# Optimization experiments

Measured on AMD Instinct MI355X. Metric: run time of the kernel, lower is better.

The kernel has to match this reference:

```python
import jax, jax.numpy as jnp
import numpy as np

SR = 24000
BLOCK = 0.4
OVERLAP = 0.7
FRAME = int(BLOCK * SR)                # 9600
SHIFT = int(BLOCK * SR * (1 - OVERLAP))
GAMMA_A = -70.0
ALPHA = 1e-4
EPS = 1e-8


def measure_loudness(sig):
    # sig: [N, T] flattened (batch*bands) envelope signals
    N, T = sig.shape
    n_frames = (T - FRAME) // SHIFT + 1
    # unfold: overlapping windows [n_frames, FRAME] of sample indices
    win_idx = jnp.arange(n_frames)[:, None] * SHIFT + jnp.arange(FRAME)[None, :]
    # mean-square energy per window (== sum(x^2)/frame_size in torch) -> [N, n_frames]
    z = jnp.mean(sig[:, win_idx] ** 2, axis=-1)
    el = -0.691 + 10.0 * jnp.log10(z + EPS)
    # absolute gating
    idx_a = (el > GAMMA_A).astype(z.dtype)
    z_ave_a = jnp.sum(z * idx_a, axis=1, keepdims=True) / (jnp.sum(idx_a, axis=1, keepdims=True) + EPS)
    # relative gating 10 dB below gated loudness
    gamma_r = -0.691 + 10.0 * jnp.log10(z_ave_a + EPS) - 10.0
    idx_ar = idx_a * (el > gamma_r).astype(z.dtype)
    z_ave_ar = jnp.sum(z * idx_ar, axis=1, keepdims=True) / (jnp.sum(idx_ar, axis=1, keepdims=True) + EPS)
    lufs = -0.691 + 10.0 * jnp.log10(z_ave_ar + EPS)  # [N, 1]
    return lufs


def setup_inputs() -> dict:
    key = jax.random.key(0)
    k1, k2 = jax.random.split(key)
    B, C, T = 16, 32, 192000  # batch, auditory bands, 8 s @ 24 kHz
    x_env = 0.1 * jax.random.normal(k1, (B, C, T), dtype=jnp.float32)
    y_env = 0.1 * jax.random.normal(k2, (B, C, T), dtype=jnp.float32)
    return {"x_env": x_env, "y_env": y_env}


def reference(x_env, y_env):
    B, C, T = x_env.shape
    loud_x = measure_loudness(x_env.reshape(B * C, T))
    loud_y = measure_loudness(y_env.reshape(B * C, T))
    level_loss = ALPHA * jnp.sum(jnp.maximum(loud_y - loud_x, 0.0))
    return level_loss
```

## Files before the change

### kernel.cpp

```cpp
#include <hip/hip_runtime.h>

constexpr int T_LEN    = 192000;
constexpr int N_SIG    = 512;
constexpr int FRAME    = 9600;
constexpr int SHIFT    = 2880;
constexpr int SUB      = 960;
constexpr int NFRAMES  = (T_LEN - FRAME) / SHIFT + 1;
constexpr int SUB_PER_SHIFT = SHIFT / SUB;
constexpr int SUB_PER_FRAME = FRAME / SUB;
constexpr int NSUB     = (NFRAMES - 1) * SUB_PER_SHIFT + SUB_PER_FRAME;
constexpr int F4_PER_SUB = SUB / 4;

typedef float f32x4 __attribute__((ext_vector_type(4)));

__device__ __forceinline__ float wave_reduce_f32(float v) {
    #pragma unroll
    for (int off = 32; off > 0; off >>= 1) v += __shfl_xor(v, off);
    return v;
}

__device__ __forceinline__ double wave_reduce_f64(double v) {
    #pragma unroll
    for (int off = 32; off > 0; off >>= 1) v += __shfl_xor(v, off);
    return v;
}

__global__ __launch_bounds__(256) void dhaspi_loudness_kernel(
    const float* __restrict__ x, const float* __restrict__ y,
    float* __restrict__ lufs_out)
{
    const int bid  = blockIdx.x;
    const int p    = bid >> 9;
    const int n    = bid & (N_SIG - 1);
    const float* sig = (p == 0 ? x : y) + (size_t)n * T_LEN;
    const f32x4* sig4 = reinterpret_cast<const f32x4*>(sig);

    __shared__ float s_sub[NSUB];

    const int tid  = threadIdx.x;
    const int wave = tid >> 6;
    const int lane = tid & 63;

    for (int k = wave; k < NSUB; k += 4) {
        float acc = 0.0f;
        const int base = k * F4_PER_SUB;
        #pragma unroll
        for (int i = 0; i < 4; ++i) {
            int idx = i * 64 + lane;
            if (idx < F4_PER_SUB) {
                f32x4 v = __builtin_nontemporal_load(&sig4[base + idx]);
                acc += v.x * v.x + v.y * v.y + v.z * v.z + v.w * v.w;
            }
        }
        acc = wave_reduce_f32(acc);
        if (lane == 0) s_sub[k] = acc;
    }
    __syncthreads();

    if (wave == 0) {
        float zs = 0.0f;
        const int b0 = lane * SUB_PER_SHIFT;
        #pragma unroll
        for (int j = 0; j < SUB_PER_FRAME; ++j) zs += s_sub[b0 + j];
        const double z  = (double)zs / (double)FRAME;
        const double el = -0.691 + 10.0 * log10(z + 1e-8);

        const double ia = (el > -70.0) ? 1.0 : 0.0;
        double sz = wave_reduce_f64(z * ia);
        double si = wave_reduce_f64(ia);
        const double z_ave_a = sz / (si + 1e-8);

        const double gamma_r = -0.691 + 10.0 * log10(z_ave_a + 1e-8) - 10.0;
        const double iar = ia * ((el > gamma_r) ? 1.0 : 0.0);
        double sz2 = wave_reduce_f64(z * iar);
        double si2 = wave_reduce_f64(iar);
        const double z_ave_ar = sz2 / (si2 + 1e-8);

        const double lufs = -0.691 + 10.0 * log10(z_ave_ar + 1e-8);
        if (lane == 0) lufs_out[bid] = (float)lufs;
    }
}

__global__ __launch_bounds__(512) void dhaspi_loss_kernel(
    const float* __restrict__ lufs, float* __restrict__ out)
{
    const int tid  = threadIdx.x;
    const int wave = tid >> 6;
    const int lane = tid & 63;

    const float lx = lufs[tid];
    const float ly = lufs[N_SIG + tid];
    const float d  = ly - lx;
    double v = (d > 0.0f) ? (double)d : 0.0;
    v = wave_reduce_f64(v);

    __shared__ double s[8];
    if (lane == 0) s[wave] = v;
    __syncthreads();
    if (tid == 0) {
        double t = 0.0;
        #pragma unroll
        for (int i = 0; i < 8; ++i) t += s[i];
        out[0] = (float)(1e-4 * t);
    }
}

extern "C" void kernel_launch(void* const* d_in, const int* in_sizes, int n_in,
                              void* d_out, int out_size, void* d_ws, size_t ws_size,
                              hipStream_t stream) {
    const float* x = (const float*)d_in[0];
    const float* y = (const float*)d_in[1];
    float* lufs = (float*)d_ws;
    float* out  = (float*)d_out;

    dhaspi_loudness_kernel<<<2 * N_SIG, 256, 0, stream>>>(x, y, lufs);
    dhaspi_loss_kernel<<<1, 512, 0, stream>>>(lufs, out);
}
```

Measured before the change: 120.2 us.

## Fuse loudness and loss kernels with last-block atomic reduction

Merges the per-signal loudness kernel and the final hinge-sum kernel into one launch. Each 512-thread block handles both the x and y signal for one index, so the grid is 512 blocks instead of 1024. The last block to finish, found through an atomic counter, does the final reduction. This removes one kernel launch and the intermediate lufs round-trip, but adds a memset launch and halves the block count, which may cut parallelism across CUs.

```diff
diff --git a/kernel.cpp b/kernel.cpp
--- a/kernel.cpp
+++ b/kernel.cpp
@@ -10,6 +10,7 @@
 constexpr int SUB_PER_FRAME = FRAME / SUB;
 constexpr int NSUB     = (NFRAMES - 1) * SUB_PER_SHIFT + SUB_PER_FRAME;
 constexpr int F4_PER_SUB = SUB / 4;
+constexpr int NWAVES   = 8;
 
 typedef float f32x4 __attribute__((ext_vector_type(4)));
 
@@ -25,23 +26,10 @@
     return v;
 }
 
-__global__ __launch_bounds__(256) void dhaspi_loudness_kernel(
-    const float* __restrict__ x, const float* __restrict__ y,
-    float* __restrict__ lufs_out)
+__device__ double block_lufs(const f32x4* __restrict__ sig4,
+                             int wave, int lane, float* s_sub)
 {
-    const int bid  = blockIdx.x;
-    const int p    = bid >> 9;
-    const int n    = bid & (N_SIG - 1);
-    const float* sig = (p == 0 ? x : y) + (size_t)n * T_LEN;
-    const f32x4* sig4 = reinterpret_cast<const f32x4*>(sig);
-
-    __shared__ float s_sub[NSUB];
-
-    const int tid  = threadIdx.x;
-    const int wave = tid >> 6;
-    const int lane = tid & 63;
-
-    for (int k = wave; k < NSUB; k += 4) {
+    for (int k = wave; k < NSUB; k += NWAVES) {
         float acc = 0.0f;
         const int base = k * F4_PER_SUB;
         #pragma unroll
@@ -57,6 +45,7 @@
     }
     __syncthreads();
 
+    double lufs = 0.0;
     if (wave == 0) {
         float zs = 0.0f;
         const int b0 = lane * SUB_PER_SHIFT;
@@ -76,32 +65,56 @@
         double si2 = wave_reduce_f64(iar);
         const double z_ave_ar = sz2 / (si2 + 1e-8);
 
-        const double lufs = -0.691 + 10.0 * log10(z_ave_ar + 1e-8);
-        if (lane == 0) lufs_out[bid] = (float)lufs;
+        lufs = -0.691 + 10.0 * log10(z_ave_ar + 1e-8);
     }
+    __syncthreads();
+    return lufs;
 }
 
-__global__ __launch_bounds__(512) void dhaspi_loss_kernel(
-    const float* __restrict__ lufs, float* __restrict__ out)
+__global__ __launch_bounds__(512) void dhaspi_fused_kernel(
+    const float* __restrict__ x, const float* __restrict__ y,
+    double* __restrict__ hinge_ws,
+    unsigned int* __restrict__ cnt,
+    float* __restrict__ out)
 {
+    const int n    = blockIdx.x;
     const int tid  = threadIdx.x;
     const int wave = tid >> 6;
     const int lane = tid & 63;
 
-    const float lx = lufs[tid];
-    const float ly = lufs[N_SIG + tid];
-    const float d  = ly - lx;
-    double v = (d > 0.0f) ? (double)d : 0.0;
-    v = wave_reduce_f64(v);
+    __shared__ float s_sub[NSUB];
+    __shared__ bool  s_win;
 
-    __shared__ double s[8];
-    if (lane == 0) s[wave] = v;
+    const f32x4* x4 = reinterpret_cast<const f32x4*>(x + (size_t)n * T_LEN);
+    const f32x4* y4 = reinterpret_cast<const f32x4*>(y + (size_t)n * T_LEN);
+
+    const double lx = block_lufs(x4, wave, lane, s_sub);
+    const double ly = block_lufs(y4, wave, lane, s_sub);
+
+    if (tid == 0) {
+        double h = ly - lx;
+        h = (h > 0.0) ? h : 0.0;
+        __hip_atomic_store(&hinge_ws[n], h, __ATOMIC_RELAXED,
+                           __HIP_MEMORY_SCOPE_AGENT);
+        unsigned int old = __hip_atomic_fetch_add(cnt, 1u, __ATOMIC_ACQ_REL,
+                                                  __HIP_MEMORY_SCOPE_AGENT);
+        s_win = (old == (unsigned int)(gridDim.x - 1));
+    }
     __syncthreads();
-    if (tid == 0) {
-        double t = 0.0;
-        #pragma unroll
-        for (int i = 0; i < 8; ++i) t += s[i];
-        out[0] = (float)(1e-4 * t);
+
+    if (s_win) {
+        double v = __hip_atomic_load(&hinge_ws[tid], __ATOMIC_RELAXED,
+                                     __HIP_MEMORY_SCOPE_AGENT);
+        v = wave_reduce_f64(v);
+        __shared__ double sd[NWAVES];
+        if (lane == 0) sd[wave] = v;
+        __syncthreads();
+        if (tid == 0) {
+            double t = 0.0;
+            #pragma unroll
+            for (int i = 0; i < NWAVES; ++i) t += sd[i];
+            out[0] = (float)(1e-4 * t);
+        }
     }
 }
 
@@ -110,9 +123,11 @@
                               hipStream_t stream) {
     const float* x = (const float*)d_in[0];
     const float* y = (const float*)d_in[1];
-    float* lufs = (float*)d_ws;
-    float* out  = (float*)d_out;
+    float* out = (float*)d_out;
 
-    dhaspi_loudness_kernel<<<2 * N_SIG, 256, 0, stream>>>(x, y, lufs);
-    dhaspi_loss_kernel<<<1, 512, 0, stream>>>(lufs, out);
+    double* hinge_ws = (double*)d_ws;
+    unsigned int* cnt = (unsigned int*)((char*)d_ws + N_SIG * sizeof(double));
+
+    hipMemsetAsync(cnt, 0, sizeof(unsigned int), stream);
+    dhaspi_fused_kernel<<<N_SIG, 512, 0, stream>>>(x, y, hinge_ws, cnt, out);
 }
```

Measured after the change: 143.7 us. 1.2x slower.
